# Performance work log

Hardware: AMD Instinct MI355X
Metric: run time of the kernel (lower is better)

## Reference

```python
import jax, jax.numpy as jnp
import numpy as np

PATCH = 3  # patch_size
PAD = PATCH // 2


def _unfold(x, p, pad):
    """torch F.unfold(x, kernel_size=p, padding=pad, stride=1) -> [B, H*W, C*p*p].

    Channel ordering matches torch: (c, kh, kw) flattened c-major.
    """
    B, C, H, W = x.shape
    xp = jnp.pad(x, ((0, 0), (0, 0), (pad, pad), (pad, pad)))
    # fixed small loop over p*p kernel offsets (9 for p=3)
    slices = [xp[:, :, i:i + H, j:j + W] for i in range(p) for j in range(p)]
    patches = jnp.stack(slices, axis=2)              # [B, C, p*p, H, W]
    patches = patches.reshape(B, C * p * p, H * W)   # c-major like torch unfold
    return patches.transpose(0, 2, 1)                # [B, H*W, C*p*p]


def setup_inputs() -> dict:
    key = jax.random.key(0)
    k1, k2 = jax.random.split(key)
    B, C, H, W = 16, 64, 64, 64
    num_memories = 512
    mem_dim = C * PATCH * PATCH  # 576
    x = jax.random.normal(k1, (B, C, H, W), dtype=jnp.float32)
    memory = jax.random.normal(k2, (num_memories, mem_dim), dtype=jnp.float32)
    temperature = jnp.ones((1,), dtype=jnp.float32) * 10.0
    return {"x": x, "memory": memory, "temperature": temperature}


def reference(x, memory, temperature):
    B, C, H, W = x.shape
    mem_dim = memory.shape[1]
    x_unfold = _unfold(x, PATCH, PAD)                      # [B, HW, D]
    scale = 1.0 / jnp.sqrt(jnp.float32(mem_dim))
    # similarity_type == 'dot'
    sim = jnp.einsum('bnd,md->bnm', x_unfold, memory) * scale * temperature[0]
    att = jax.nn.softmax(sim, axis=2)                      # [B, HW, M]
    read_out = jnp.einsum('bnm,md->bnd', att, memory)      # [B, HW, D]
    return read_out
```

## Files before the change

kernel.cpp:

```cpp
#include <hip/hip_runtime.h>

typedef _Float16 half8 __attribute__((ext_vector_type(8)));
typedef float floatx4 __attribute__((ext_vector_type(4)));
typedef int intx4 __attribute__((ext_vector_type(4)));

#define MFMA16(a, b, c) __builtin_amdgcn_mfma_f32_16x16x32_f16(a, b, c, 0, 0, 0)

static __device__ __forceinline__ half8 asH8(intx4 v) {
  half8 r;
  __builtin_memcpy(&r, &v, 16);
  return r;
}

static constexpr int kD = 576;
static constexpr int WS2T = 589824;

__global__ void prep_split(const float* __restrict__ mem,
                           const float* __restrict__ temperature,
                           _Float16* __restrict__ ws) {
  const int m = blockIdx.x;
  const int d = threadIdx.x;
  const float sfac = temperature[0] * 0.060112293370373475f;
  float v = mem[m * kD + d];
  const int kt = d >> 5;
  ws[kt * 16384 + m * 32 + (d & 31)] = (_Float16)(v * sfac);
  ws[WS2T + (m >> 5) * 18432 + d * 32 + (m & 31)] = (_Float16)v;
}

#define GLD16A(dst, base, voff)                              \
  asm volatile("global_load_dwordx4 %0, %1, %2 offset:0"     \
               : "=v"(dst)                                   \
               : "v"(voff), "s"(base))
#define VMW(N)                                            \
  do {                                                    \
    asm volatile("s_waitcnt vmcnt(" #N ")" ::: "memory"); \
    __builtin_amdgcn_sched_barrier(0);                    \
  } while (0)

__global__ __launch_bounds__(512, 2) void mem_branch_kernel(
    const float* __restrict__ x, const float* __restrict__ temperature,
    const _Float16* __restrict__ ws, float* __restrict__ out) {
  __shared__ __align__(16) unsigned char blob[77824];
  _Float16* afrag = (_Float16*)blob;
  int* tab = (int*)(blob + 73728);
  float* reds = (float*)(blob + 73728);

  const int tid = threadIdx.x;
  const int lane = tid & 63;
  const int wv = tid >> 6;
  const int l15 = lane & 15;
  const int koct = lane >> 4;
  const int bx = blockIdx.x;
  const int b = bx >> 6;
  const int h = bx & 63;

  const _Float16* wsp = ws;
  const _Float16* wsp2 = ws + WS2T;

  for (int d = tid; d < kD; d += 512) {
    int c = d / 9, r9 = d % 9, kh = r9 / 3, kw = r9 % 3;
    tab[d] = (c << 12) + (kh << 6) + kw + (kh << 20) + (kw << 24);
  }
  __syncthreads();

  {
    const int base0 = (b * 4096 + (h - 1)) * 64 - 1;
    for (int i = 0; i < 9; ++i) {
      const int combo = i * 8 + wv;
      const int pt = combo & 3;
      const int kt = combo >> 2;
      const int pp = pt * 16 + l15;
      const int dbase = kt * 32 + koct * 8;
      intx4 t0 = *reinterpret_cast<const intx4*>(&tab[dbase]);
      intx4 t1 = *reinterpret_cast<const intx4*>(&tab[dbase + 4]);
      half8 hv;
#pragma unroll
      for (int j = 0; j < 8; ++j) {
        int t = (j < 4) ? t0[j] : t1[j - 4];
        int off = t & 0xFFFFF;
        int kh = (t >> 20) & 15;
        int kw = (t >> 24) & 15;
        bool ok = ((unsigned)(h - 1 + kh) < 64u) && ((unsigned)(pp - 1 + kw) < 64u);
        int idx = ok ? (base0 + pp + off) : 0;
        float v = x[idx];
        v = ok ? v : 0.0f;
        hv[j] = (_Float16)v;
      }
      *reinterpret_cast<half8*>(&afrag[combo * 512 + lane * 8]) = hv;
    }
  }
  __syncthreads();

  const _Float16* abase = afrag + lane * 8;

  floatx4 acc[4][4];
  const floatx4 zed = {0.0f, 0.0f, 0.0f, 0.0f};
#pragma unroll
  for (int pt = 0; pt < 4; ++pt)
#pragma unroll
    for (int mt = 0; mt < 4; ++mt) acc[pt][mt] = zed;
  {
    int vb[4];
#pragma unroll
    for (int mt = 0; mt < 4; ++mt) vb[mt] = (wv * 64 + mt * 16 + l15) * 64 + koct * 16;
    intx4 U0, U1, U2, U3, V0, V1, V2, V3, W0, W1, W2, W3, X0, X1, X2, X3;
    half8 aa0, aa1, aa2, aa3;
    int aoff = 0;

#define G1_ISSUE(B, KIO)              \
  do {                                \
    GLD16A(B##0, wsp, vb[0] + (KIO)); \
    GLD16A(B##1, wsp, vb[1] + (KIO)); \
    GLD16A(B##2, wsp, vb[2] + (KIO)); \
    GLD16A(B##3, wsp, vb[3] + (KIO)); \
  } while (0)

#define G1_AREAD                                                \
  do {                                                          \
    aa0 = *reinterpret_cast<const half8*>(abase + aoff);        \
    aa1 = *reinterpret_cast<const half8*>(abase + aoff + 512);  \
    aa2 = *reinterpret_cast<const half8*>(abase + aoff + 1024); \
    aa3 = *reinterpret_cast<const half8*>(abase + aoff + 1536); \
    aoff += 2048;                                               \
  } while (0)

#define G1_MMA(B)                                   \
  do {                                              \
    __builtin_amdgcn_s_setprio(1);                  \
    acc[0][0] = MFMA16(aa0, asH8(B##0), acc[0][0]); \
    acc[1][0] = MFMA16(aa1, asH8(B##0), acc[1][0]); \
    acc[2][0] = MFMA16(aa2, asH8(B##0), acc[2][0]); \
    acc[3][0] = MFMA16(aa3, asH8(B##0), acc[3][0]); \
    acc[0][1] = MFMA16(aa0, asH8(B##1), acc[0][1]); \
    acc[1][1] = MFMA16(aa1, asH8(B##1), acc[1][1]); \
    acc[2][1] = MFMA16(aa2, asH8(B##1), acc[2][1]); \
    acc[3][1] = MFMA16(aa3, asH8(B##1), acc[3][1]); \
    acc[0][2] = MFMA16(aa0, asH8(B##2), acc[0][2]); \
    acc[1][2] = MFMA16(aa1, asH8(B##2), acc[1][2]); \
    acc[2][2] = MFMA16(aa2, asH8(B##2), acc[2][2]); \
    acc[3][2] = MFMA16(aa3, asH8(B##2), acc[3][2]); \
    acc[0][3] = MFMA16(aa0, asH8(B##3), acc[0][3]); \
    acc[1][3] = MFMA16(aa1, asH8(B##3), acc[1][3]); \
    acc[2][3] = MFMA16(aa2, asH8(B##3), acc[2][3]); \
    acc[3][3] = MFMA16(aa3, asH8(B##3), acc[3][3]); \
    __builtin_amdgcn_s_setprio(0);                  \
  } while (0)

    G1_ISSUE(U, 0);
    G1_ISSUE(V, 32768);
    G1_ISSUE(W, 65536);
    for (int g = 0; g < 3; ++g) {
      const int j3 = (4 * g + 3) * 32768;
      const int j4 = j3 + 32768, j5 = j4 + 32768, j6 = j5 + 32768;
      G1_ISSUE(X, j3); G1_AREAD; VMW(12); G1_MMA(U);
      G1_ISSUE(U, j4); G1_AREAD; VMW(12); G1_MMA(V);
      G1_ISSUE(V, j5); G1_AREAD; VMW(12); G1_MMA(W);
      G1_ISSUE(W, j6); G1_AREAD; VMW(12); G1_MMA(X);
    }
    G1_ISSUE(X, 15 * 32768); G1_AREAD; VMW(12); G1_MMA(U);
    G1_ISSUE(U, 16 * 32768); G1_AREAD; VMW(12); G1_MMA(V);
    G1_ISSUE(V, 17 * 32768); G1_AREAD; VMW(12); G1_MMA(W);
    G1_AREAD; VMW(8); G1_MMA(X);
    G1_AREAD; VMW(4); G1_MMA(U);
    G1_AREAD; VMW(0); G1_MMA(V);
  }

  float ps[4][4];
#pragma unroll
  for (int pt = 0; pt < 4; ++pt)
#pragma unroll
    for (int r = 0; r < 4; ++r) ps[pt][r] = 0.0f;
#pragma unroll
  for (int pt = 0; pt < 4; ++pt)
#pragma unroll
    for (int mt = 0; mt < 4; ++mt)
#pragma unroll
      for (int r = 0; r < 4; ++r) {
        float e = exp2f(acc[pt][mt][r]);
        acc[pt][mt][r] = e;
        ps[pt][r] += e;
      }
#pragma unroll
  for (int off = 1; off < 16; off <<= 1)
#pragma unroll
    for (int pt = 0; pt < 4; ++pt)
#pragma unroll
      for (int r = 0; r < 4; ++r) ps[pt][r] += __shfl_xor(ps[pt][r], off, 64);
  if (l15 == 0) {
#pragma unroll
    for (int pt = 0; pt < 4; ++pt)
#pragma unroll
      for (int r = 0; r < 4; ++r) reds[wv * 64 + pt * 16 + koct * 4 + r] = ps[pt][r];
  }
  __syncthreads();
#pragma unroll
  for (int pt = 0; pt < 4; ++pt)
#pragma unroll
    for (int r = 0; r < 4; ++r) {
      const int p = pt * 16 + koct * 4 + r;
      float s = reds[p];
#pragma unroll
      for (int w = 1; w < 8; ++w) s += reds[w * 64 + p];
      ps[pt][r] = 1.0f / s;
    }
#pragma unroll
  for (int pt = 0; pt < 4; ++pt)
#pragma unroll
    for (int mt = 0; mt < 4; ++mt)
#pragma unroll
      for (int r = 0; r < 4; ++r) {
        float a = acc[pt][mt][r] * ps[pt][r];
        const int m = wv * 64 + mt * 16 + l15;
        const int idxe =
            (((m >> 5) * 4 + pt) * 64 + ((m >> 3) & 3) * 16 + koct * 4 + r) * 8 + (m & 7);
        afrag[idxe] = (_Float16)a;
      }
  __syncthreads();

  floatx4 acc2[5][4];
#pragma unroll
  for (int nt = 0; nt < 5; ++nt)
#pragma unroll
    for (int pt = 0; pt < 4; ++pt) acc2[nt][pt] = zed;

#define G2_AREAD                                                \
  do {                                                          \
    p0 = *reinterpret_cast<const half8*>(abase + aoff2);        \
    p1 = *reinterpret_cast<const half8*>(abase + aoff2 + 512);  \
    p2 = *reinterpret_cast<const half8*>(abase + aoff2 + 1024); \
    p3 = *reinterpret_cast<const half8*>(abase + aoff2 + 1536); \
    aoff2 += 2048;                                              \
  } while (0)

  if (wv < 4) {
    int vc[5];
#pragma unroll
    for (int nt = 0; nt < 5; ++nt) vc[nt] = ((wv * 5 + nt) * 16 + l15) * 64 + koct * 16;
    intx4 Ta0, Ta1, Ta2, Ta3, Ta4;
    intx4 Tb0, Tb1, Tb2, Tb3, Tb4;
    intx4 Tc0, Tc1, Tc2, Tc3, Tc4;
    intx4 Td0, Td1, Td2, Td3, Td4;
    half8 p0, p1, p2, p3;
    int aoff2 = 0;

#define G2_ISSUE5(B, KIO)              \
  do {                                 \
    GLD16A(B##0, wsp2, vc[0] + (KIO)); \
    GLD16A(B##1, wsp2, vc[1] + (KIO)); \
    GLD16A(B##2, wsp2, vc[2] + (KIO)); \
    GLD16A(B##3, wsp2, vc[3] + (KIO)); \
    GLD16A(B##4, wsp2, vc[4] + (KIO)); \
  } while (0)

#define G2_MMA5(B)                                   \
  do {                                               \
    __builtin_amdgcn_s_setprio(1);                   \
    acc2[0][0] = MFMA16(p0, asH8(B##0), acc2[0][0]); \
    acc2[0][1] = MFMA16(p1, asH8(B##0), acc2[0][1]); \
    acc2[0][2] = MFMA16(p2, asH8(B##0), acc2[0][2]); \
    acc2[0][3] = MFMA16(p3, asH8(B##0), acc2[0][3]); \
    acc2[1][0] = MFMA16(p0, asH8(B##1), acc2[1][0]); \
    acc2[1][1] = MFMA16(p1, asH8(B##1), acc2[1][1]); \
    acc2[1][2] = MFMA16(p2, asH8(B##1), acc2[1][2]); \
    acc2[1][3] = MFMA16(p3, asH8(B##1), acc2[1][3]); \
    acc2[2][0] = MFMA16(p0, asH8(B##2), acc2[2][0]); \
    acc2[2][1] = MFMA16(p1, asH8(B##2), acc2[2][1]); \
    acc2[2][2] = MFMA16(p2, asH8(B##2), acc2[2][2]); \
    acc2[2][3] = MFMA16(p3, asH8(B##2), acc2[2][3]); \
    acc2[3][0] = MFMA16(p0, asH8(B##3), acc2[3][0]); \
    acc2[3][1] = MFMA16(p1, asH8(B##3), acc2[3][1]); \
    acc2[3][2] = MFMA16(p2, asH8(B##3), acc2[3][2]); \
    acc2[3][3] = MFMA16(p3, asH8(B##3), acc2[3][3]); \
    acc2[4][0] = MFMA16(p0, asH8(B##4), acc2[4][0]); \
    acc2[4][1] = MFMA16(p1, asH8(B##4), acc2[4][1]); \
    acc2[4][2] = MFMA16(p2, asH8(B##4), acc2[4][2]); \
    acc2[4][3] = MFMA16(p3, asH8(B##4), acc2[4][3]); \
    __builtin_amdgcn_s_setprio(0);                   \
  } while (0)

    G2_ISSUE5(Ta, 0);
    G2_ISSUE5(Tb, 36864);
    G2_ISSUE5(Tc, 73728);
    for (int g = 0; g < 3; ++g) {
      const int j3 = (4 * g + 3) * 36864, j4 = j3 + 36864, j5 = j4 + 36864, j6 = j5 + 36864;
      G2_ISSUE5(Td, j3); G2_AREAD; VMW(15); G2_MMA5(Ta);
      G2_ISSUE5(Ta, j4); G2_AREAD; VMW(15); G2_MMA5(Tb);
      G2_ISSUE5(Tb, j5); G2_AREAD; VMW(15); G2_MMA5(Tc);
      G2_ISSUE5(Tc, j6); G2_AREAD; VMW(15); G2_MMA5(Td);
    }
    G2_ISSUE5(Td, 15 * 36864); G2_AREAD; VMW(15); G2_MMA5(Ta);
    G2_AREAD; VMW(10); G2_MMA5(Tb);
    G2_AREAD; VMW(5);  G2_MMA5(Tc);
    G2_AREAD; VMW(0);  G2_MMA5(Td);

    const int nbase = b * 4096 + h * 64;
#pragma unroll
    for (int nt = 0; nt < 5; ++nt) {
      const int d = (wv * 5 + nt) * 16 + l15;
#pragma unroll
      for (int pt = 0; pt < 4; ++pt)
#pragma unroll
        for (int r = 0; r < 4; ++r) {
          const int px = pt * 16 + koct * 4 + r;
          __builtin_nontemporal_store(acc2[nt][pt][r], &out[(nbase + px) * 576 + d]);
        }
    }
  } else {
    int vc[4];
#pragma unroll
    for (int nt = 0; nt < 4; ++nt)
      vc[nt] = ((20 + (wv - 4) * 4 + nt) * 16 + l15) * 64 + koct * 16;
    intx4 Ta0, Ta1, Ta2, Ta3;
    intx4 Tb0, Tb1, Tb2, Tb3;
    intx4 Tc0, Tc1, Tc2, Tc3;
    intx4 Td0, Td1, Td2, Td3;
    half8 p0, p1, p2, p3;
    int aoff2 = 0;

#define G2_ISSUE4(B, KIO)              \
  do {                                 \
    GLD16A(B##0, wsp2, vc[0] + (KIO)); \
    GLD16A(B##1, wsp2, vc[1] + (KIO)); \
    GLD16A(B##2, wsp2, vc[2] + (KIO)); \
    GLD16A(B##3, wsp2, vc[3] + (KIO)); \
  } while (0)

#define G2_MMA4(B)                                   \
  do {                                               \
    __builtin_amdgcn_s_setprio(1);                   \
    acc2[0][0] = MFMA16(p0, asH8(B##0), acc2[0][0]); \
    acc2[0][1] = MFMA16(p1, asH8(B##0), acc2[0][1]); \
    acc2[0][2] = MFMA16(p2, asH8(B##0), acc2[0][2]); \
    acc2[0][3] = MFMA16(p3, asH8(B##0), acc2[0][3]); \
    acc2[1][0] = MFMA16(p0, asH8(B##1), acc2[1][0]); \
    acc2[1][1] = MFMA16(p1, asH8(B##1), acc2[1][1]); \
    acc2[1][2] = MFMA16(p2, asH8(B##1), acc2[1][2]); \
    acc2[1][3] = MFMA16(p3, asH8(B##1), acc2[1][3]); \
    acc2[2][0] = MFMA16(p0, asH8(B##2), acc2[2][0]); \
    acc2[2][1] = MFMA16(p1, asH8(B##2), acc2[2][1]); \
    acc2[2][2] = MFMA16(p2, asH8(B##2), acc2[2][2]); \
    acc2[2][3] = MFMA16(p3, asH8(B##2), acc2[2][3]); \
    acc2[3][0] = MFMA16(p0, asH8(B##3), acc2[3][0]); \
    acc2[3][1] = MFMA16(p1, asH8(B##3), acc2[3][1]); \
    acc2[3][2] = MFMA16(p2, asH8(B##3), acc2[3][2]); \
    acc2[3][3] = MFMA16(p3, asH8(B##3), acc2[3][3]); \
    __builtin_amdgcn_s_setprio(0);                   \
  } while (0)

    G2_ISSUE4(Ta, 0);
    G2_ISSUE4(Tb, 36864);
    G2_ISSUE4(Tc, 73728);
    for (int g = 0; g < 3; ++g) {
      const int j3 = (4 * g + 3) * 36864, j4 = j3 + 36864, j5 = j4 + 36864, j6 = j5 + 36864;
      G2_ISSUE4(Td, j3); G2_AREAD; VMW(12); G2_MMA4(Ta);
      G2_ISSUE4(Ta, j4); G2_AREAD; VMW(12); G2_MMA4(Tb);
      G2_ISSUE4(Tb, j5); G2_AREAD; VMW(12); G2_MMA4(Tc);
      G2_ISSUE4(Tc, j6); G2_AREAD; VMW(12); G2_MMA4(Td);
    }
    G2_ISSUE4(Td, 15 * 36864); G2_AREAD; VMW(12); G2_MMA4(Ta);
    G2_AREAD; VMW(8); G2_MMA4(Tb);
    G2_AREAD; VMW(4); G2_MMA4(Tc);
    G2_AREAD; VMW(0); G2_MMA4(Td);

    const int nbase = b * 4096 + h * 64;
#pragma unroll
    for (int nt = 0; nt < 4; ++nt) {
      const int d = (20 + (wv - 4) * 4 + nt) * 16 + l15;
#pragma unroll
      for (int pt = 0; pt < 4; ++pt)
#pragma unroll
        for (int r = 0; r < 4; ++r) {
          const int px = pt * 16 + koct * 4 + r;
          __builtin_nontemporal_store(acc2[nt][pt][r], &out[(nbase + px) * 576 + d]);
        }
    }
  }
}

extern "C" void kernel_launch(void* const* d_in, const int* in_sizes, int n_in,
                              void* d_out, int out_size, void* d_ws, size_t ws_size,
                              hipStream_t stream) {
  const float* x = (const float*)d_in[0];
  const float* memory = (const float*)d_in[1];
  const float* temperature = (const float*)d_in[2];
  float* out = (float*)d_out;
  _Float16* ws = (_Float16*)d_ws;

  prep_split<<<512, 576, 0, stream>>>(memory, temperature, ws);
  mem_branch_kernel<<<1024, 512, 0, stream>>>(x, temperature, ws, out);
}
```

Before: 134.1 us.

## Prefetch first two GEMM2 memory tiles into LDS during softmax

Issues global-to-LDS async loads for the first two k-steps of the second GEMM's memory operand before the softmax phase, so their latency overlaps the exp/reduction work. The GEMM2 pipeline then starts from LDS-staged tiles and streams the rest through registers as before. LDS grows from about 76 KB to 156 KB per block, which could cut blocks per CU below the launch-bounds target of two.

Result: no change. 132.4 us (-1.3%).

```diff
diff --git a/kernel.cpp b/kernel.cpp
--- a/kernel.cpp
+++ b/kernel.cpp
@@ -36,11 +36,15 @@
     asm volatile("s_waitcnt vmcnt(" #N ")" ::: "memory"); \
     __builtin_amdgcn_sched_barrier(0);                    \
   } while (0)
+#define GLD_LDS16(gp, lp)                                                          \
+  __builtin_amdgcn_global_load_lds((__attribute__((address_space(1))) void*)(gp),  \
+                                   (__attribute__((address_space(3))) void*)(lp),  \
+                                   16, 0, 0)
 
 __global__ __launch_bounds__(512, 2) void mem_branch_kernel(
     const float* __restrict__ x, const float* __restrict__ temperature,
     const _Float16* __restrict__ ws, float* __restrict__ out) {
-  __shared__ __align__(16) unsigned char blob[77824];
+  __shared__ __align__(16) unsigned char blob[159744];
   _Float16* afrag = (_Float16*)blob;
   int* tab = (int*)(blob + 73728);
   float* reds = (float*)(blob + 73728);
@@ -56,6 +60,8 @@
 
   const _Float16* wsp = ws;
   const _Float16* wsp2 = ws + WS2T;
+  const unsigned char* wsb2 = (const unsigned char*)wsp2;
+  unsigned char* stg = blob + 77824 + wv * 10240;
 
   for (int d = tid; d < kD; d += 512) {
     int c = d / 9, r9 = d % 9, kh = r9 / 3, kw = r9 % 3;
@@ -92,6 +98,17 @@
   __syncthreads();
 
   const _Float16* abase = afrag + lane * 8;
+
+  int vc5[5];
+  if (wv < 4) {
+#pragma unroll
+    for (int nt = 0; nt < 5; ++nt) vc5[nt] = ((wv * 5 + nt) * 16 + l15) * 64 + koct * 16;
+  } else {
+#pragma unroll
+    for (int nt = 0; nt < 4; ++nt)
+      vc5[nt] = ((20 + (wv - 4) * 4 + nt) * 16 + l15) * 64 + koct * 16;
+    vc5[4] = vc5[3];
+  }
 
   floatx4 acc[4][4];
   const floatx4 zed = {0.0f, 0.0f, 0.0f, 0.0f};
@@ -165,6 +182,20 @@
     G1_AREAD; VMW(0); G1_MMA(V);
   }
 
+  if (wv < 4) {
+#pragma unroll
+    for (int nt = 0; nt < 5; ++nt) GLD_LDS16(wsb2 + vc5[nt], stg + nt * 1024);
+#pragma unroll
+    for (int nt = 0; nt < 5; ++nt)
+      GLD_LDS16(wsb2 + vc5[nt] + 36864, stg + 5120 + nt * 1024);
+  } else {
+#pragma unroll
+    for (int nt = 0; nt < 4; ++nt) GLD_LDS16(wsb2 + vc5[nt], stg + nt * 1024);
+#pragma unroll
+    for (int nt = 0; nt < 4; ++nt)
+      GLD_LDS16(wsb2 + vc5[nt] + 36864, stg + 5120 + nt * 1024);
+  }
+
   float ps[4][4];
 #pragma unroll
   for (int pt = 0; pt < 4; ++pt)
@@ -233,9 +264,6 @@
   } while (0)
 
   if (wv < 4) {
-    int vc[5];
-#pragma unroll
-    for (int nt = 0; nt < 5; ++nt) vc[nt] = ((wv * 5 + nt) * 16 + l15) * 64 + koct * 16;
     intx4 Ta0, Ta1, Ta2, Ta3, Ta4;
     intx4 Tb0, Tb1, Tb2, Tb3, Tb4;
     intx4 Tc0, Tc1, Tc2, Tc3, Tc4;
@@ -243,13 +271,13 @@
     half8 p0, p1, p2, p3;
     int aoff2 = 0;
 
-#define G2_ISSUE5(B, KIO)              \
-  do {                                 \
-    GLD16A(B##0, wsp2, vc[0] + (KIO)); \
-    GLD16A(B##1, wsp2, vc[1] + (KIO)); \
-    GLD16A(B##2, wsp2, vc[2] + (KIO)); \
-    GLD16A(B##3, wsp2, vc[3] + (KIO)); \
-    GLD16A(B##4, wsp2, vc[4] + (KIO)); \
+#define G2_ISSUE5(B, KIO)               \
+  do {                                  \
+    GLD16A(B##0, wsp2, vc5[0] + (KIO)); \
+    GLD16A(B##1, wsp2, vc5[1] + (KIO)); \
+    GLD16A(B##2, wsp2, vc5[2] + (KIO)); \
+    GLD16A(B##3, wsp2, vc5[3] + (KIO)); \
+    GLD16A(B##4, wsp2, vc5[4] + (KIO)); \
   } while (0)
 
 #define G2_MMA5(B)                                   \
@@ -278,20 +306,56 @@
     __builtin_amdgcn_s_setprio(0);                   \
   } while (0)
 
-    G2_ISSUE5(Ta, 0);
-    G2_ISSUE5(Tb, 36864);
-    G2_ISSUE5(Tc, 73728);
-    for (int g = 0; g < 3; ++g) {
-      const int j3 = (4 * g + 3) * 36864, j4 = j3 + 36864, j5 = j4 + 36864, j6 = j5 + 36864;
-      G2_ISSUE5(Td, j3); G2_AREAD; VMW(15); G2_MMA5(Ta);
-      G2_ISSUE5(Ta, j4); G2_AREAD; VMW(15); G2_MMA5(Tb);
-      G2_ISSUE5(Tb, j5); G2_AREAD; VMW(15); G2_MMA5(Tc);
-      G2_ISSUE5(Tc, j6); G2_AREAD; VMW(15); G2_MMA5(Td);
-    }
-    G2_ISSUE5(Td, 15 * 36864); G2_AREAD; VMW(15); G2_MMA5(Ta);
-    G2_AREAD; VMW(10); G2_MMA5(Tb);
-    G2_AREAD; VMW(5);  G2_MMA5(Tc);
-    G2_AREAD; VMW(0);  G2_MMA5(Td);
+#define G2_SMMA5(POFF)                                                                 \
+  do {                                                                                 \
+    const half8 s0 = *reinterpret_cast<const half8*>(stg + (POFF) + lane * 16);        \
+    const half8 s1 = *reinterpret_cast<const half8*>(stg + (POFF) + 1024 + lane * 16); \
+    const half8 s2 = *reinterpret_cast<const half8*>(stg + (POFF) + 2048 + lane * 16); \
+    const half8 s3 = *reinterpret_cast<const half8*>(stg + (POFF) + 3072 + lane * 16); \
+    const half8 s4 = *reinterpret_cast<const half8*>(stg + (POFF) + 4096 + lane * 16); \
+    __builtin_amdgcn_s_setprio(1);                                                     \
+    acc2[0][0] = MFMA16(p0, s0, acc2[0][0]);                                           \
+    acc2[0][1] = MFMA16(p1, s0, acc2[0][1]);                                           \
+    acc2[0][2] = MFMA16(p2, s0, acc2[0][2]);                                           \
+    acc2[0][3] = MFMA16(p3, s0, acc2[0][3]);                                           \
+    acc2[1][0] = MFMA16(p0, s1, acc2[1][0]);                                           \
+    acc2[1][1] = MFMA16(p1, s1, acc2[1][1]);                                           \
+    acc2[1][2] = MFMA16(p2, s1, acc2[1][2]);                                           \
+    acc2[1][3] = MFMA16(p3, s1, acc2[1][3]);                                           \
+    acc2[2][0] = MFMA16(p0, s2, acc2[2][0]);                                           \
+    acc2[2][1] = MFMA16(p1, s2, acc2[2][1]);                                           \
+    acc2[2][2] = MFMA16(p2, s2, acc2[2][2]);                                           \
+    acc2[2][3] = MFMA16(p3, s2, acc2[2][3]);                                           \
+    acc2[3][0] = MFMA16(p0, s3, acc2[3][0]);                                           \
+    acc2[3][1] = MFMA16(p1, s3, acc2[3][1]);                                           \
+    acc2[3][2] = MFMA16(p2, s3, acc2[3][2]);                                           \
+    acc2[3][3] = MFMA16(p3, s3, acc2[3][3]);                                           \
+    acc2[4][0] = MFMA16(p0, s4, acc2[4][0]);                                           \
+    acc2[4][1] = MFMA16(p1, s4, acc2[4][1]);                                           \
+    acc2[4][2] = MFMA16(p2, s4, acc2[4][2]);                                           \
+    acc2[4][3] = MFMA16(p3, s4, acc2[4][3]);                                           \
+    __builtin_amdgcn_s_setprio(0);                                                     \
+  } while (0)
+
+    G2_ISSUE5(Ta, 2 * 36864);
+    G2_ISSUE5(Tb, 3 * 36864);
+    G2_ISSUE5(Tc, 4 * 36864);
+    G2_AREAD; G2_SMMA5(0);
+    G2_AREAD; G2_SMMA5(5120);
+    for (int g = 0; g < 2; ++g) {
+      const int j0 = (4 * g + 5) * 36864;
+      const int j1 = j0 + 36864, j2 = j1 + 36864, j3 = j2 + 36864;
+      G2_ISSUE5(Td, j0); G2_AREAD; VMW(15); G2_MMA5(Ta);
+      G2_ISSUE5(Ta, j1); G2_AREAD; VMW(15); G2_MMA5(Tb);
+      G2_ISSUE5(Tb, j2); G2_AREAD; VMW(15); G2_MMA5(Tc);
+      G2_ISSUE5(Tc, j3); G2_AREAD; VMW(15); G2_MMA5(Td);
+    }
+    G2_ISSUE5(Td, 13 * 36864); G2_AREAD; VMW(15); G2_MMA5(Ta);
+    G2_ISSUE5(Ta, 14 * 36864); G2_AREAD; VMW(15); G2_MMA5(Tb);
+    G2_ISSUE5(Tb, 15 * 36864); G2_AREAD; VMW(15); G2_MMA5(Tc);
+    G2_AREAD; VMW(10); G2_MMA5(Td);
+    G2_AREAD; VMW(5);  G2_MMA5(Ta);
+    G2_AREAD; VMW(0);  G2_MMA5(Tb);
 
     const int nbase = b * 4096 + h * 64;
 #pragma unroll
@@ -306,10 +370,6 @@
         }
     }
   } else {
-    int vc[4];
-#pragma unroll
-    for (int nt = 0; nt < 4; ++nt)
-      vc[nt] = ((20 + (wv - 4) * 4 + nt) * 16 + l15) * 64 + koct * 16;
     intx4 Ta0, Ta1, Ta2, Ta3;
     intx4 Tb0, Tb1, Tb2, Tb3;
     intx4 Tc0, Tc1, Tc2, Tc3;
@@ -317,12 +377,12 @@
     half8 p0, p1, p2, p3;
     int aoff2 = 0;
 
-#define G2_ISSUE4(B, KIO)              \
-  do {                                 \
-    GLD16A(B##0, wsp2, vc[0] + (KIO)); \
-    GLD16A(B##1, wsp2, vc[1] + (KIO)); \
-    GLD16A(B##2, wsp2, vc[2] + (KIO)); \
-    GLD16A(B##3, wsp2, vc[3] + (KIO)); \
+#define G2_ISSUE4(B, KIO)               \
+  do {                                  \
+    GLD16A(B##0, wsp2, vc5[0] + (KIO)); \
+    GLD16A(B##1, wsp2, vc5[1] + (KIO)); \
+    GLD16A(B##2, wsp2, vc5[2] + (KIO)); \
+    GLD16A(B##3, wsp2, vc5[3] + (KIO)); \
   } while (0)
 
 #define G2_MMA4(B)                                   \
@@ -347,20 +407,51 @@
     __builtin_amdgcn_s_setprio(0);                   \
   } while (0)
 
-    G2_ISSUE4(Ta, 0);
-    G2_ISSUE4(Tb, 36864);
-    G2_ISSUE4(Tc, 73728);
-    for (int g = 0; g < 3; ++g) {
-      const int j3 = (4 * g + 3) * 36864, j4 = j3 + 36864, j5 = j4 + 36864, j6 = j5 + 36864;
-      G2_ISSUE4(Td, j3); G2_AREAD; VMW(12); G2_MMA4(Ta);
-      G2_ISSUE4(Ta, j4); G2_AREAD; VMW(12); G2_MMA4(Tb);
-      G2_ISSUE4(Tb, j5); G2_AREAD; VMW(12); G2_MMA4(Tc);
-      G2_ISSUE4(Tc, j6); G2_AREAD; VMW(12); G2_MMA4(Td);
-    }
-    G2_ISSUE4(Td, 15 * 36864); G2_AREAD; VMW(12); G2_MMA4(Ta);
-    G2_AREAD; VMW(8); G2_MMA4(Tb);
-    G2_AREAD; VMW(4); G2_MMA4(Tc);
-    G2_AREAD; VMW(0); G2_MMA4(Td);
+#define G2_SMMA4(POFF)                                                                 \
+  do {                                                                                 \
+    const half8 s0 = *reinterpret_cast<const half8*>(stg + (POFF) + lane * 16);        \
+    const half8 s1 = *reinterpret_cast<const half8*>(stg + (POFF) + 1024 + lane * 16); \
+    const half8 s2 = *reinterpret_cast<const half8*>(stg + (POFF) + 2048 + lane * 16); \
+    const half8 s3 = *reinterpret_cast<const half8*>(stg + (POFF) + 3072 + lane * 16); \
+    __builtin_amdgcn_s_setprio(1);                                                     \
+    acc2[0][0] = MFMA16(p0, s0, acc2[0][0]);                                           \
+    acc2[0][1] = MFMA16(p1, s0, acc2[0][1]);                                           \
+    acc2[0][2] = MFMA16(p2, s0, acc2[0][2]);                                           \
+    acc2[0][3] = MFMA16(p3, s0, acc2[0][3]);                                           \
+    acc2[1][0] = MFMA16(p0, s1, acc2[1][0]);                                           \
+    acc2[1][1] = MFMA16(p1, s1, acc2[1][1]);                                           \
+    acc2[1][2] = MFMA16(p2, s1, acc2[1][2]);                                           \
+    acc2[1][3] = MFMA16(p3, s1, acc2[1][3]);                                           \
+    acc2[2][0] = MFMA16(p0, s2, acc2[2][0]);                                           \
+    acc2[2][1] = MFMA16(p1, s2, acc2[2][1]);                                           \
+    acc2[2][2] = MFMA16(p2, s2, acc2[2][2]);                                           \
+    acc2[2][3] = MFMA16(p3, s2, acc2[2][3]);                                           \
+    acc2[3][0] = MFMA16(p0, s3, acc2[3][0]);                                           \
+    acc2[3][1] = MFMA16(p1, s3, acc2[3][1]);                                           \
+    acc2[3][2] = MFMA16(p2, s3, acc2[3][2]);                                           \
+    acc2[3][3] = MFMA16(p3, s3, acc2[3][3]);                                           \
+    __builtin_amdgcn_s_setprio(0);                                                     \
+  } while (0)
+
+    G2_ISSUE4(Ta, 2 * 36864);
+    G2_ISSUE4(Tb, 3 * 36864);
+    G2_ISSUE4(Tc, 4 * 36864);
+    G2_AREAD; G2_SMMA4(0);
+    G2_AREAD; G2_SMMA4(5120);
+    for (int g = 0; g < 2; ++g) {
+      const int j0 = (4 * g + 5) * 36864;
+      const int j1 = j0 + 36864, j2 = j1 + 36864, j3 = j2 + 36864;
+      G2_ISSUE4(Td, j0); G2_AREAD; VMW(12); G2_MMA4(Ta);
+      G2_ISSUE4(Ta, j1); G2_AREAD; VMW(12); G2_MMA4(Tb);
+      G2_ISSUE4(Tb, j2); G2_AREAD; VMW(12); G2_MMA4(Tc);
+      G2_ISSUE4(Tc, j3); G2_AREAD; VMW(12); G2_MMA4(Td);
+    }
+    G2_ISSUE4(Td, 13 * 36864); G2_AREAD; VMW(12); G2_MMA4(Ta);
+    G2_ISSUE4(Ta, 14 * 36864); G2_AREAD; VMW(12); G2_MMA4(Tb);
+    G2_ISSUE4(Tb, 15 * 36864); G2_AREAD; VMW(12); G2_MMA4(Tc);
+    G2_AREAD; VMW(8); G2_MMA4(Td);
+    G2_AREAD; VMW(4); G2_MMA4(Ta);
+    G2_AREAD; VMW(0); G2_MMA4(Tb);
 
     const int nbase = b * 4096 + h * 64;
 #pragma unroll
```
